# Optimization experiments

Measured on AMD Instinct MI355X. Metric: run time of the kernel, lower is better.

The kernel has to match this reference:

```python
import jax, jax.numpy as jnp
import numpy as np


def setup_inputs() -> dict:
    key = jax.random.key(0)
    k1, k2, k3, k4, k5 = jax.random.split(key, 5)
    B, S, T = 256, 512, 64
    emissions = jax.random.normal(k1, (B, S, T), dtype=jnp.float32)
    tags = jax.random.randint(k2, (B, S), 0, T, dtype=jnp.int64)
    mask = jnp.ones((B, S), dtype=jnp.int32)
    init_range = 0.1
    start_transitions = jax.random.uniform(k3, (T,), minval=-init_range, maxval=init_range, dtype=jnp.float32)
    end_transitions = jax.random.uniform(k4, (T,), minval=-init_range, maxval=init_range, dtype=jnp.float32)
    transitions = jax.random.uniform(k5, (T, T), minval=-init_range, maxval=init_range, dtype=jnp.float32)
    return {"emissions": emissions, "tags": tags, "mask": mask,
            "start_transitions": start_transitions,
            "end_transitions": end_transitions,
            "transitions": transitions}


def _crf_nll_mean(emissions, tags, mask, start_transitions, end_transitions, transitions):
    # batch_first -> time-major: [S, B, T], [S, B]
    em = jnp.transpose(emissions, (1, 0, 2))
    tg = jnp.transpose(tags, (1, 0))
    mk = jnp.transpose(mask, (1, 0))
    maskf = mk.astype(em.dtype)                      # [S, B]
    S, B, T = em.shape
    batch_idx = jnp.arange(B)

    # ---- numerator: score of the gold path (fully vectorized) ----
    emit = jnp.take_along_axis(em, tg[:, :, None], axis=2)[..., 0]   # [S, B]
    trans_sc = transitions[tg[:-1], tg[1:]]                          # [S-1, B]
    score_num = start_transitions[tg[0]] + emit[0]
    score_num = score_num + jnp.sum((trans_sc + emit[1:]) * maskf[1:], axis=0)
    seq_ends = jnp.sum(mk, axis=0) - 1                               # [B]
    last_tags = tg[seq_ends, batch_idx]
    score_num = score_num + end_transitions[last_tags]

    # ---- denominator: log-partition via logsumexp scan ----
    init = start_transitions + em[0]                                 # [B, T]

    def step(score, xs):
        em_i, m_i = xs                                               # [B,T], [B]
        # [B, T_prev, T_next]
        next_score = score[:, :, None] + transitions[None, :, :] + em_i[:, None, :]
        next_score = jax.nn.logsumexp(next_score, axis=1)
        score = jnp.where(m_i[:, None] != 0, next_score, score)
        return score, None

    final, _ = jax.lax.scan(step, init, (em[1:], mk[1:]))
    denom = jax.nn.logsumexp(final + end_transitions, axis=1)        # [B]

    llh = denom - score_num                                          # [B]
    return jnp.mean(llh)                                             # reduction='mean'


def reference(emissions, tags, mask, start_transitions, end_transitions, transitions):
    return _crf_nll_mean(emissions, tags, mask, start_transitions, end_transitions, transitions)
```

## Files before the change

### kernel.cpp

```cpp
#include <hip/hip_runtime.h>
#include <hip/hip_bf16.h>

#define BATCH 256
#define SEQ   512
#define NT    64
#define PCH   12
#define CLEN  43
#define PITCH 68

typedef __attribute__((ext_vector_type(8)))  short bf16x8;
typedef __attribute__((ext_vector_type(16))) float f32x16;
typedef __attribute__((ext_vector_type(4)))  float f32x4;

#define MEMBAR() __asm__ __volatile__("" ::: "memory")

static __device__ __forceinline__ short bf16_trunc(float v) {
    return (short)(__float_as_uint(v) >> 16);
}
static __device__ __forceinline__ unsigned pack_bf16_rn(float lo, float hi) {
    float2 f; f.x = lo; f.y = hi;
    __hip_bfloat162 h = __float22bfloat162_rn(f);
    unsigned u; __builtin_memcpy(&u, &h, 4);
    return u;
}

__global__ __launch_bounds__(64, 2) void crf_chunk_kernel(
    const float* __restrict__ emissions,
    const int*   __restrict__ tags,
    const int*   __restrict__ mask,
    const float* __restrict__ start_tr,
    const float* __restrict__ trans,
    unsigned short* __restrict__ mats,
    float* __restrict__ ws_head,
    float* __restrict__ score_part,
    int*   __restrict__ mcnt_part)
{
    __shared__ __align__(16) unsigned char smem[CLEN * NT * 4];
    float (*w_lds)[NT] = (float (*)[NT])smem;
    unsigned short* ldsT = (unsigned short*)smem;

    const int c    = blockIdx.x;
    const int b    = blockIdx.y;
    const int lane = threadIdx.x;
    const int h    = lane >> 5;
    const int ml   = lane & 31;

    if (c == 0 && b == 0 && lane == 0) {
        ws_head[0] = 0.f;
        ((unsigned*)ws_head)[1] = 0u;
    }

    const int s0 = c * CLEN;
    int L = (SEQ - 1) - s0; if (L > CLEN) L = CLEN;

    const float* em_b = emissions + (size_t)b * SEQ * NT;
    const int*   tg_b = tags + b * SEQ;
    const int*   mk_b = mask + b * SEQ;

    for (int s = 0; s < L; ++s)
        w_lds[s][lane] = __expf(em_b[(size_t)(s0 + 1 + s) * NT + lane]);

    float np = 0.f;
    int   mc = 0;
    if (lane < L) {
        int s  = s0 + 1 + lane;
        int m  = mk_b[s];
        mc = m;
        int t  = tg_b[s];
        int tp = tg_b[s - 1];
        float v = trans[tp * NT + t] + em_b[(size_t)s * NT + t];
        np = m ? v : 0.f;
    }
    if (c == 0 && lane == 0) {
        int t0 = tg_b[0];
        np += start_tr[t0] + em_b[t0];
        mc += mk_b[0];
    }
#pragma unroll
    for (int d = 32; d; d >>= 1) {
        np += __shfl_xor(np, d);
        mc += __shfl_xor(mc, d);
    }
    if (lane == 0) {
        score_part[b * PCH + c] = np;
        mcnt_part[b * PCH + c]  = mc;
    }

    bf16x8 Af[2][4];
#pragma unroll
    for (int mt = 0; mt < 2; ++mt) {
        int m = mt * 32 + ml;
#pragma unroll
        for (int kk = 0; kk < 4; ++kk) {
            bf16x8 f;
#pragma unroll
            for (int j = 0; j < 8; ++j) {
                int r = 32 * (kk >> 1) + 16 * (kk & 1) + (j & 3) + 8 * (j >> 2) + 4 * h;
                f[j] = bf16_trunc(__expf(trans[r * NT + m]) * 0.0078125f);
            }
            Af[mt][kk] = f;
        }
    }

    union BU { unsigned u[4]; bf16x8 v; };
    BU Bv[4][2];
#pragma unroll
    for (int kk = 0; kk < 4; ++kk)
#pragma unroll
        for (int nt = 0; nt < 2; ++nt) {
            int n = nt * 32 + ml;
#pragma unroll
            for (int d = 0; d < 4; ++d) {
                int j0 = 2 * d;
                int r0 = 32 * (kk >> 1) + 16 * (kk & 1) + (j0 & 3) + 8 * (j0 >> 2) + 4 * h;
                unsigned lo = (r0     == n) ? 0x3f80u : 0u;
                unsigned hi = (r0 + 1 == n) ? 0x3f80u : 0u;
                Bv[kk][nt].u[d] = lo | (hi << 16);
            }
        }

    __syncthreads();

    const f32x16 zf = {};

    for (int s = 0; s < L; ++s) {
        f32x4 wq[4][2];
#pragma unroll
        for (int kk = 0; kk < 4; ++kk) {
            int base = 32 * (kk >> 1) + 16 * (kk & 1) + 4 * h;
            wq[kk][0] = *(const f32x4*)&w_lds[s][base];
            wq[kk][1] = *(const f32x4*)&w_lds[s][base + 8];
        }

        f32x16 acc[2][2];
#pragma unroll
        for (int mt = 0; mt < 2; ++mt)
#pragma unroll
            for (int nt = 0; nt < 2; ++nt) {
                f32x16 a = __builtin_amdgcn_mfma_f32_32x32x16_bf16(Af[mt][0], Bv[0][nt].v, zf, 0, 0, 0);
                a = __builtin_amdgcn_mfma_f32_32x32x16_bf16(Af[mt][1], Bv[1][nt].v, a, 0, 0, 0);
                a = __builtin_amdgcn_mfma_f32_32x32x16_bf16(Af[mt][2], Bv[2][nt].v, a, 0, 0, 0);
                a = __builtin_amdgcn_mfma_f32_32x32x16_bf16(Af[mt][3], Bv[3][nt].v, a, 0, 0, 0);
                acc[mt][nt] = a;
            }

#pragma unroll
        for (int kk = 0; kk < 4; ++kk) {
            const int mt_s = kk >> 1, qo = 8 * (kk & 1);
#pragma unroll
            for (int nt = 0; nt < 2; ++nt) {
#pragma unroll
                for (int d = 0; d < 4; ++d) {
                    int j0 = 2 * d;
                    float v0 = acc[mt_s][nt][qo + j0]     * wq[kk][d >> 1][2 * (d & 1)];
                    float v1 = acc[mt_s][nt][qo + j0 + 1] * wq[kk][d >> 1][2 * (d & 1) + 1];
                    Bv[kk][nt].u[d] = pack_bf16_rn(v0, v1);
                }
            }
        }
    }

    __threadfence_block();
#pragma unroll
    for (int kk = 0; kk < 4; ++kk)
#pragma unroll
        for (int nt = 0; nt < 2; ++nt) {
            int n = nt * 32 + ml;
#pragma unroll
            for (int d = 0; d < 4; ++d) {
                int j0 = 2 * d;
                int r0 = 32 * (kk >> 1) + 16 * (kk & 1) + (j0 & 3) + 8 * (j0 >> 2) + 4 * h;
                *(unsigned*)&ldsT[n * PITCH + r0] = Bv[kk][nt].u[d];
            }
        }
    __threadfence_block();

    unsigned short* outp = mats + ((size_t)(b * PCH + c)) * 4096;
    for (int it = 0; it < 8; ++it) {
        int o = it * 512 + lane * 8;
        int n = o >> 6, k = o & 63;
        const uint2* p = (const uint2*)(ldsT + n * PITCH + k);
        uint2 x = p[0], y = p[1];
        uint4 q4; q4.x = x.x; q4.y = x.y; q4.z = y.x; q4.w = y.y;
        *(uint4*)(outp + o) = q4;
    }
}

__global__ __launch_bounds__(64) void crf_combine_kernel(
    const float* __restrict__ emissions,
    const int*   __restrict__ tags,
    const float* __restrict__ start_tr,
    const float* __restrict__ end_tr,
    const unsigned short* __restrict__ mats,
    const float* __restrict__ score_part,
    const int*   __restrict__ mcnt_part,
    float* __restrict__ ws_head,
    float* __restrict__ out)
{
    __shared__ __align__(16) float r_lds[NT];

    const int b = blockIdx.x;
    const int j = threadIdx.x;

    const float* em_b = emissions + (size_t)b * SEQ * NT;
    const int*   tg_b = tags + b * SEQ;
    const unsigned short* mb = mats + (size_t)b * PCH * 4096;

    float sp = (j < PCH) ? score_part[b * PCH + j] : 0.f;
    int   mp = (j < PCH) ? mcnt_part[b * PCH + j] : 0;

    float r = __expf(end_tr[j]);
    r_lds[j] = r;
    MEMBAR();
    int X = 0;

    uint4 buf[3][8];
#pragma unroll
    for (int u = 0; u < 8; ++u)
        buf[0][u] = *(const uint4*)(mb + (size_t)(PCH - 1) * 4096 + j * 64 + u * 8);
#pragma unroll
    for (int u = 0; u < 8; ++u)
        buf[1][u] = *(const uint4*)(mb + (size_t)(PCH - 2) * 4096 + j * 64 + u * 8);

#pragma unroll
    for (int d = 32; d; d >>= 1) {
        sp += __shfl_xor(sp, d);
        mp += __shfl_xor(mp, d);
    }
    int last_tag = tg_b[mp - 1];
    float score_num = sp + end_tr[last_tag];

#pragma unroll
    for (int c = PCH - 1; c >= 0; --c) {
        const int slot  = (PCH - 1 - c) % 3;
        const int nslot = (PCH - 1 - c + 2) % 3;
        if (c >= 2) {
#pragma unroll
            for (int u = 0; u < 8; ++u)
                buf[nslot][u] = *(const uint4*)(mb + (size_t)(c - 2) * 4096 + j * 64 + u * 8);
        }
        float a0 = 0.f, a1 = 0.f, a2 = 0.f, a3 = 0.f;
#pragma unroll
        for (int u = 0; u < 8; ++u) {
            uint4 q = buf[slot][u];
            f32x4 ra = *(const f32x4*)&r_lds[u * 8];
            f32x4 rb = *(const f32x4*)&r_lds[u * 8 + 4];
            a0 = fmaf(ra[0], __uint_as_float(q.x << 16),         a0);
            a1 = fmaf(ra[1], __uint_as_float(q.x & 0xffff0000u), a1);
            a2 = fmaf(ra[2], __uint_as_float(q.y << 16),         a2);
            a3 = fmaf(ra[3], __uint_as_float(q.y & 0xffff0000u), a3);
            a0 = fmaf(rb[0], __uint_as_float(q.z << 16),         a0);
            a1 = fmaf(rb[1], __uint_as_float(q.z & 0xffff0000u), a1);
            a2 = fmaf(rb[2], __uint_as_float(q.w << 16),         a2);
            a3 = fmaf(rb[3], __uint_as_float(q.w & 0xffff0000u), a3);
        }
        float rn = (a0 + a1) + (a2 + a3);
        unsigned eb = (__builtin_amdgcn_readfirstlane((int)__float_as_uint(rn)) >> 23) & 0xffu;
        r = rn * __uint_as_float((254u - eb) << 23);
        X += (int)eb - 127;
        MEMBAR();
        r_lds[j] = r;
        MEMBAR();
    }

    float u0 = __expf(start_tr[j] + em_b[j]);
    float v = r * u0;
#pragma unroll
    for (int d = 32; d; d >>= 1) v += __shfl_xor(v, d);

    if (j == 0) {
        float denom = __logf(v) + (float)(X + 7 * (SEQ - 1)) * 0.6931471805599453f;
        float llh = denom - score_num;
        atomicAdd(&ws_head[0], llh * (1.0f / BATCH));
        __threadfence();
        unsigned old = atomicAdd((unsigned*)ws_head + 1, 1u);
        if (old == BATCH - 1) {
            __threadfence();
            out[0] = atomicAdd(&ws_head[0], 0.0f);
        }
    }
}

extern "C" void kernel_launch(void* const* d_in, const int* in_sizes, int n_in,
                              void* d_out, int out_size, void* d_ws, size_t ws_size,
                              hipStream_t stream) {
    const float* emissions = (const float*)d_in[0];
    const int*   tags      = (const int*)d_in[1];
    const int*   mask      = (const int*)d_in[2];
    const float* start_tr  = (const float*)d_in[3];
    const float* end_tr    = (const float*)d_in[4];
    const float* trans     = (const float*)d_in[5];

    float* ws_head    = (float*)d_ws;
    float* score_part = (float*)((char*)d_ws + 64);
    int*   mcnt_part  = (int*)((char*)d_ws + 64 + 4 * BATCH * PCH);
    unsigned short* mats = (unsigned short*)((char*)d_ws + 32768);

    crf_chunk_kernel<<<dim3(PCH, BATCH), 64, 0, stream>>>(
        emissions, tags, mask, start_tr, trans, mats, ws_head, score_part, mcnt_part);
    crf_combine_kernel<<<BATCH, 64, 0, stream>>>(
        emissions, tags, start_tr, end_tr, mats, score_part, mcnt_part,
        ws_head, (float*)d_out);
}
```

Measured before the change: 166.8 us.

## Fuse chunk and combine kernels via last-block atomic, split columns across two waves

Merges the per-chunk matrix-product kernel and the combine kernel into one launch. The last block to finish for each batch row, detected with an atomic counter that a memset clears, does the combine. Each block now runs two waves, each owning half the output columns, which halves the serial MFMA chain per wave. Chunk count drops from 12 to 8 with longer chunks. This removes a kernel launch and boundary, but the dependent chain per block gets longer, and it adds a memset plus global fences.

```diff
diff --git a/kernel.cpp b/kernel.cpp
--- a/kernel.cpp
+++ b/kernel.cpp
@@ -4,13 +4,13 @@
 #define BATCH 256
 #define SEQ   512
 #define NT    64
-#define PCH   12
-#define CLEN  43
+#define PCH   8
+#define CLEN  64
 #define PITCH 68
 
-typedef __attribute__((ext_vector_type(8)))  short bf16x8;
-typedef __attribute__((ext_vector_type(16))) float f32x16;
-typedef __attribute__((ext_vector_type(4)))  float f32x4;
+typedef short bf16x8  __attribute__((ext_vector_type(8)));
+typedef float f32x16  __attribute__((ext_vector_type(16)));
+typedef float f32x4   __attribute__((ext_vector_type(4)));
 
 #define MEMBAR() __asm__ __volatile__("" ::: "memory")
 
@@ -19,36 +19,38 @@
 }
 static __device__ __forceinline__ unsigned pack_bf16_rn(float lo, float hi) {
     float2 f; f.x = lo; f.y = hi;
-    __hip_bfloat162 h = __float22bfloat162_rn(f);
-    unsigned u; __builtin_memcpy(&u, &h, 4);
+    __hip_bfloat162 hh = __float22bfloat162_rn(f);
+    unsigned u; __builtin_memcpy(&u, &hh, 4);
     return u;
 }
 
-__global__ __launch_bounds__(64, 2) void crf_chunk_kernel(
+__global__ __launch_bounds__(128, 4) void crf_fused_kernel(
     const float* __restrict__ emissions,
     const int*   __restrict__ tags,
     const int*   __restrict__ mask,
     const float* __restrict__ start_tr,
+    const float* __restrict__ end_tr,
     const float* __restrict__ trans,
     unsigned short* __restrict__ mats,
     float* __restrict__ ws_head,
+    unsigned* __restrict__ done,
     float* __restrict__ score_part,
-    int*   __restrict__ mcnt_part)
+    int*   __restrict__ mcnt_part,
+    float* __restrict__ out)
 {
     __shared__ __align__(16) unsigned char smem[CLEN * NT * 4];
+    __shared__ unsigned is_last;
     float (*w_lds)[NT] = (float (*)[NT])smem;
     unsigned short* ldsT = (unsigned short*)smem;
+    float* r_lds = (float*)smem;
 
     const int c    = blockIdx.x;
     const int b    = blockIdx.y;
-    const int lane = threadIdx.x;
+    const int tid  = threadIdx.x;
+    const int lane = tid & 63;
+    const int wave = tid >> 6;
     const int h    = lane >> 5;
     const int ml   = lane & 31;
-
-    if (c == 0 && b == 0 && lane == 0) {
-        ws_head[0] = 0.f;
-        ((unsigned*)ws_head)[1] = 0u;
-    }
 
     const int s0 = c * CLEN;
     int L = (SEQ - 1) - s0; if (L > CLEN) L = CLEN;
@@ -57,33 +59,35 @@
     const int*   tg_b = tags + b * SEQ;
     const int*   mk_b = mask + b * SEQ;
 
-    for (int s = 0; s < L; ++s)
-        w_lds[s][lane] = __expf(em_b[(size_t)(s0 + 1 + s) * NT + lane]);
-
-    float np = 0.f;
-    int   mc = 0;
-    if (lane < L) {
-        int s  = s0 + 1 + lane;
-        int m  = mk_b[s];
-        mc = m;
-        int t  = tg_b[s];
-        int tp = tg_b[s - 1];
-        float v = trans[tp * NT + t] + em_b[(size_t)s * NT + t];
-        np = m ? v : 0.f;
-    }
-    if (c == 0 && lane == 0) {
-        int t0 = tg_b[0];
-        np += start_tr[t0] + em_b[t0];
-        mc += mk_b[0];
-    }
-#pragma unroll
-    for (int d = 32; d; d >>= 1) {
-        np += __shfl_xor(np, d);
-        mc += __shfl_xor(mc, d);
-    }
-    if (lane == 0) {
-        score_part[b * PCH + c] = np;
-        mcnt_part[b * PCH + c]  = mc;
+    for (int i = tid; i < L * NT; i += 128)
+        ((float*)smem)[i] = __expf(em_b[(size_t)(s0 + 1) * NT + i]);
+
+    if (wave == 0) {
+        float np = 0.f;
+        int   mc = 0;
+        if (lane < L) {
+            int s  = s0 + 1 + lane;
+            int m  = mk_b[s];
+            mc = m;
+            int t  = tg_b[s];
+            int tp = tg_b[s - 1];
+            float v = trans[tp * NT + t] + em_b[(size_t)s * NT + t];
+            np = m ? v : 0.f;
+        }
+        if (c == 0 && lane == 0) {
+            int t0 = tg_b[0];
+            np += start_tr[t0] + em_b[t0];
+            mc += mk_b[0];
+        }
+#pragma unroll
+        for (int d = 32; d; d >>= 1) {
+            np += __shfl_xor(np, d);
+            mc += __shfl_xor(mc, d);
+        }
+        if (lane == 0) {
+            score_part[b * PCH + c] = np;
+            mcnt_part[b * PCH + c]  = mc;
+        }
     }
 
     bf16x8 Af[2][4];
@@ -103,141 +107,116 @@
     }
 
     union BU { unsigned u[4]; bf16x8 v; };
-    BU Bv[4][2];
+    BU Bv[4];
+    const int n_own = wave * 32 + ml;
 #pragma unroll
     for (int kk = 0; kk < 4; ++kk)
 #pragma unroll
-        for (int nt = 0; nt < 2; ++nt) {
-            int n = nt * 32 + ml;
+        for (int d = 0; d < 4; ++d) {
+            int j0 = 2 * d;
+            int r0 = 32 * (kk >> 1) + 16 * (kk & 1) + (j0 & 3) + 8 * (j0 >> 2) + 4 * h;
+            unsigned lo = (r0     == n_own) ? 0x3f80u : 0u;
+            unsigned hi = (r0 + 1 == n_own) ? 0x3f80u : 0u;
+            Bv[kk].u[d] = lo | (hi << 16);
+        }
+
+    __syncthreads();
+
+    for (int s = 0; s < L; ++s) {
+        f32x4 wq0[4], wq1[4];
+#pragma unroll
+        for (int kk = 0; kk < 4; ++kk) {
+            int base = 32 * (kk >> 1) + 16 * (kk & 1) + 4 * h;
+            wq0[kk] = *(const f32x4*)&w_lds[s][base];
+            wq1[kk] = *(const f32x4*)&w_lds[s][base + 8];
+        }
+
+        const f32x16 zf = {};
+        f32x16 a0 = __builtin_amdgcn_mfma_f32_32x32x16_bf16(Af[0][0], Bv[0].v, zf, 0, 0, 0);
+        a0 = __builtin_amdgcn_mfma_f32_32x32x16_bf16(Af[0][1], Bv[1].v, a0, 0, 0, 0);
+        a0 = __builtin_amdgcn_mfma_f32_32x32x16_bf16(Af[0][2], Bv[2].v, a0, 0, 0, 0);
+        a0 = __builtin_amdgcn_mfma_f32_32x32x16_bf16(Af[0][3], Bv[3].v, a0, 0, 0, 0);
+        f32x16 a1 = __builtin_amdgcn_mfma_f32_32x32x16_bf16(Af[1][0], Bv[0].v, zf, 0, 0, 0);
+        a1 = __builtin_amdgcn_mfma_f32_32x32x16_bf16(Af[1][1], Bv[1].v, a1, 0, 0, 0);
+        a1 = __builtin_amdgcn_mfma_f32_32x32x16_bf16(Af[1][2], Bv[2].v, a1, 0, 0, 0);
+        a1 = __builtin_amdgcn_mfma_f32_32x32x16_bf16(Af[1][3], Bv[3].v, a1, 0, 0, 0);
+
+#pragma unroll
+        for (int kk = 0; kk < 4; ++kk) {
+            const int qo = 8 * (kk & 1);
 #pragma unroll
             for (int d = 0; d < 4; ++d) {
                 int j0 = 2 * d;
-                int r0 = 32 * (kk >> 1) + 16 * (kk & 1) + (j0 & 3) + 8 * (j0 >> 2) + 4 * h;
-                unsigned lo = (r0     == n) ? 0x3f80u : 0u;
-                unsigned hi = (r0 + 1 == n) ? 0x3f80u : 0u;
-                Bv[kk][nt].u[d] = lo | (hi << 16);
+                float c0 = (kk < 2) ? a0[qo + j0]     : a1[qo + j0];
+                float c1 = (kk < 2) ? a0[qo + j0 + 1] : a1[qo + j0 + 1];
+                float w0 = (d < 2) ? wq0[kk][2 * (d & 1)]     : wq1[kk][2 * (d & 1)];
+                float w1 = (d < 2) ? wq0[kk][2 * (d & 1) + 1] : wq1[kk][2 * (d & 1) + 1];
+                Bv[kk].u[d] = pack_bf16_rn(c0 * w0, c1 * w1);
             }
         }
-
-    __syncthreads();
-
-    const f32x16 zf = {};
-
-    for (int s = 0; s < L; ++s) {
-        f32x4 wq[4][2];
-#pragma unroll
-        for (int kk = 0; kk < 4; ++kk) {
-            int base = 32 * (kk >> 1) + 16 * (kk & 1) + 4 * h;
-            wq[kk][0] = *(const f32x4*)&w_lds[s][base];
-            wq[kk][1] = *(const f32x4*)&w_lds[s][base + 8];
-        }
-
-        f32x16 acc[2][2];
-#pragma unroll
-        for (int mt = 0; mt < 2; ++mt)
-#pragma unroll
-            for (int nt = 0; nt < 2; ++nt) {
-                f32x16 a = __builtin_amdgcn_mfma_f32_32x32x16_bf16(Af[mt][0], Bv[0][nt].v, zf, 0, 0, 0);
-                a = __builtin_amdgcn_mfma_f32_32x32x16_bf16(Af[mt][1], Bv[1][nt].v, a, 0, 0, 0);
-                a = __builtin_amdgcn_mfma_f32_32x32x16_bf16(Af[mt][2], Bv[2][nt].v, a, 0, 0, 0);
-                a = __builtin_amdgcn_mfma_f32_32x32x16_bf16(Af[mt][3], Bv[3][nt].v, a, 0, 0, 0);
-                acc[mt][nt] = a;
-            }
-
-#pragma unroll
-        for (int kk = 0; kk < 4; ++kk) {
-            const int mt_s = kk >> 1, qo = 8 * (kk & 1);
-#pragma unroll
-            for (int nt = 0; nt < 2; ++nt) {
-#pragma unroll
-                for (int d = 0; d < 4; ++d) {
-                    int j0 = 2 * d;
-                    float v0 = acc[mt_s][nt][qo + j0]     * wq[kk][d >> 1][2 * (d & 1)];
-                    float v1 = acc[mt_s][nt][qo + j0 + 1] * wq[kk][d >> 1][2 * (d & 1) + 1];
-                    Bv[kk][nt].u[d] = pack_bf16_rn(v0, v1);
-                }
-            }
-        }
-    }
-
-    __threadfence_block();
+    }
+
+    __syncthreads();
 #pragma unroll
     for (int kk = 0; kk < 4; ++kk)
 #pragma unroll
-        for (int nt = 0; nt < 2; ++nt) {
-            int n = nt * 32 + ml;
-#pragma unroll
-            for (int d = 0; d < 4; ++d) {
-                int j0 = 2 * d;
-                int r0 = 32 * (kk >> 1) + 16 * (kk & 1) + (j0 & 3) + 8 * (j0 >> 2) + 4 * h;
-                *(unsigned*)&ldsT[n * PITCH + r0] = Bv[kk][nt].u[d];
-            }
-        }
-    __threadfence_block();
+        for (int d = 0; d < 4; ++d) {
+            int j0 = 2 * d;
+            int r0 = 32 * (kk >> 1) + 16 * (kk & 1) + (j0 & 3) + 8 * (j0 >> 2) + 4 * h;
+            *(unsigned*)&ldsT[n_own * PITCH + r0] = Bv[kk].u[d];
+        }
+    __syncthreads();
 
     unsigned short* outp = mats + ((size_t)(b * PCH + c)) * 4096;
-    for (int it = 0; it < 8; ++it) {
-        int o = it * 512 + lane * 8;
+    for (int it = 0; it < 4; ++it) {
+        int o = it * 1024 + tid * 8;
         int n = o >> 6, k = o & 63;
         const uint2* p = (const uint2*)(ldsT + n * PITCH + k);
         uint2 x = p[0], y = p[1];
         uint4 q4; q4.x = x.x; q4.y = x.y; q4.z = y.x; q4.w = y.y;
         *(uint4*)(outp + o) = q4;
     }
-}
-
-__global__ __launch_bounds__(64) void crf_combine_kernel(
-    const float* __restrict__ emissions,
-    const int*   __restrict__ tags,
-    const float* __restrict__ start_tr,
-    const float* __restrict__ end_tr,
-    const unsigned short* __restrict__ mats,
-    const float* __restrict__ score_part,
-    const int*   __restrict__ mcnt_part,
-    float* __restrict__ ws_head,
-    float* __restrict__ out)
-{
-    __shared__ __align__(16) float r_lds[NT];
-
-    const int b = blockIdx.x;
-    const int j = threadIdx.x;
-
-    const float* em_b = emissions + (size_t)b * SEQ * NT;
-    const int*   tg_b = tags + b * SEQ;
+
+    __threadfence();
+    __syncthreads();
+    if (tid == 0) {
+        unsigned old = atomicAdd(&done[b], 1u);
+        is_last = (old == PCH - 1) ? 1u : 0u;
+    }
+    __syncthreads();
+    if (!is_last) return;
+    __threadfence();
+    if (wave != 0) return;
+
+    const int j = lane;
     const unsigned short* mb = mats + (size_t)b * PCH * 4096;
 
     float sp = (j < PCH) ? score_part[b * PCH + j] : 0.f;
     int   mp = (j < PCH) ? mcnt_part[b * PCH + j] : 0;
 
     float r = __expf(end_tr[j]);
-    r_lds[j] = r;
-    MEMBAR();
+    MEMBAR(); r_lds[j] = r; MEMBAR();
     int X = 0;
 
-    uint4 buf[3][8];
+    uint4 buf[2][8];
 #pragma unroll
     for (int u = 0; u < 8; ++u)
         buf[0][u] = *(const uint4*)(mb + (size_t)(PCH - 1) * 4096 + j * 64 + u * 8);
-#pragma unroll
-    for (int u = 0; u < 8; ++u)
-        buf[1][u] = *(const uint4*)(mb + (size_t)(PCH - 2) * 4096 + j * 64 + u * 8);
 
 #pragma unroll
     for (int d = 32; d; d >>= 1) {
         sp += __shfl_xor(sp, d);
         mp += __shfl_xor(mp, d);
     }
-    int last_tag = tg_b[mp - 1];
-    float score_num = sp + end_tr[last_tag];
-
-#pragma unroll
-    for (int c = PCH - 1; c >= 0; --c) {
-        const int slot  = (PCH - 1 - c) % 3;
-        const int nslot = (PCH - 1 - c + 2) % 3;
-        if (c >= 2) {
+    float score_num = sp + end_tr[tg_b[mp - 1]];
+
+#pragma unroll
+    for (int cc = PCH - 1; cc >= 0; --cc) {
+        const int slot = (PCH - 1 - cc) & 1;
+        if (cc > 0) {
 #pragma unroll
             for (int u = 0; u < 8; ++u)
-                buf[nslot][u] = *(const uint4*)(mb + (size_t)(c - 2) * 4096 + j * 64 + u * 8);
+                buf[slot ^ 1][u] = *(const uint4*)(mb + (size_t)(cc - 1) * 4096 + j * 64 + u * 8);
         }
         float a0 = 0.f, a1 = 0.f, a2 = 0.f, a3 = 0.f;
 #pragma unroll
@@ -291,14 +270,14 @@
     const float* end_tr    = (const float*)d_in[4];
     const float* trans     = (const float*)d_in[5];
 
-    float* ws_head    = (float*)d_ws;
-    float* score_part = (float*)((char*)d_ws + 64);
-    int*   mcnt_part  = (int*)((char*)d_ws + 64 + 4 * BATCH * PCH);
+    float*    ws_head    = (float*)d_ws;
+    unsigned* done       = (unsigned*)((char*)d_ws + 64);
+    float*    score_part = (float*)((char*)d_ws + 4096);
+    int*      mcnt_part  = (int*)((char*)d_ws + 12288);
     unsigned short* mats = (unsigned short*)((char*)d_ws + 32768);
 
-    crf_chunk_kernel<<<dim3(PCH, BATCH), 64, 0, stream>>>(
-        emissions, tags, mask, start_tr, trans, mats, ws_head, score_part, mcnt_part);
-    crf_combine_kernel<<<BATCH, 64, 0, stream>>>(
-        emissions, tags, start_tr, end_tr, mats, score_part, mcnt_part,
-        ws_head, (float*)d_out);
-}
+    hipMemsetAsync(d_ws, 0, 4096, stream);
+    crf_fused_kernel<<<dim3(PCH, BATCH), 128, 0, stream>>>(
+        emissions, tags, mask, start_tr, end_tr, trans,
+        mats, ws_head, done, score_part, mcnt_part, (float*)d_out);
+}
```

New measurement: 300.8 us. 1.8x slower.

## Fuse chunk and combine kernels via last-block-done counter, use 8 chunks

Applied to the files above, without the earlier changes.

Merges the per-chunk transfer-matrix kernel and the combine kernel into one launch. The last chunk block of each batch row, detected with an atomic counter, performs the chain of matrix-vector products. Chunk length grows from 43 to 64, so there are 8 chunks instead of 12 and the combine chain is shorter, at the cost of longer per-block sequential work. A memset is added to zero the counters, and the combine prefetch buffer drops from triple to double.

```diff
diff --git a/kernel.cpp b/kernel.cpp
--- a/kernel.cpp
+++ b/kernel.cpp
@@ -4,13 +4,13 @@
 #define BATCH 256
 #define SEQ   512
 #define NT    64
-#define PCH   12
-#define CLEN  43
+#define PCH   8
+#define CLEN  64
 #define PITCH 68
 
-typedef __attribute__((ext_vector_type(8)))  short bf16x8;
-typedef __attribute__((ext_vector_type(16))) float f32x16;
-typedef __attribute__((ext_vector_type(4)))  float f32x4;
+typedef short bf16x8  __attribute__((ext_vector_type(8)));
+typedef float f32x16  __attribute__((ext_vector_type(16)));
+typedef float f32x4   __attribute__((ext_vector_type(4)));
 
 #define MEMBAR() __asm__ __volatile__("" ::: "memory")
 
@@ -19,25 +19,29 @@
 }
 static __device__ __forceinline__ unsigned pack_bf16_rn(float lo, float hi) {
     float2 f; f.x = lo; f.y = hi;
-    __hip_bfloat162 h = __float22bfloat162_rn(f);
-    unsigned u; __builtin_memcpy(&u, &h, 4);
+    __hip_bfloat162 hh = __float22bfloat162_rn(f);
+    unsigned u; __builtin_memcpy(&u, &hh, 4);
     return u;
 }
 
-__global__ __launch_bounds__(64, 2) void crf_chunk_kernel(
+__global__ __launch_bounds__(64, 2) void crf_fused_kernel(
     const float* __restrict__ emissions,
     const int*   __restrict__ tags,
     const int*   __restrict__ mask,
     const float* __restrict__ start_tr,
+    const float* __restrict__ end_tr,
     const float* __restrict__ trans,
     unsigned short* __restrict__ mats,
     float* __restrict__ ws_head,
+    unsigned* __restrict__ done,
     float* __restrict__ score_part,
-    int*   __restrict__ mcnt_part)
+    int*   __restrict__ mcnt_part,
+    float* __restrict__ out)
 {
     __shared__ __align__(16) unsigned char smem[CLEN * NT * 4];
     float (*w_lds)[NT] = (float (*)[NT])smem;
     unsigned short* ldsT = (unsigned short*)smem;
+    float* r_lds = (float*)smem;
 
     const int c    = blockIdx.x;
     const int b    = blockIdx.y;
@@ -45,11 +49,6 @@
     const int h    = lane >> 5;
     const int ml   = lane & 31;
 
-    if (c == 0 && b == 0 && lane == 0) {
-        ws_head[0] = 0.f;
-        ((unsigned*)ws_head)[1] = 0u;
-    }
-
     const int s0 = c * CLEN;
     int L = (SEQ - 1) - s0; if (L > CLEN) L = CLEN;
 
@@ -60,30 +59,32 @@
     for (int s = 0; s < L; ++s)
         w_lds[s][lane] = __expf(em_b[(size_t)(s0 + 1 + s) * NT + lane]);
 
-    float np = 0.f;
-    int   mc = 0;
-    if (lane < L) {
-        int s  = s0 + 1 + lane;
-        int m  = mk_b[s];
-        mc = m;
-        int t  = tg_b[s];
-        int tp = tg_b[s - 1];
-        float v = trans[tp * NT + t] + em_b[(size_t)s * NT + t];
-        np = m ? v : 0.f;
-    }
-    if (c == 0 && lane == 0) {
-        int t0 = tg_b[0];
-        np += start_tr[t0] + em_b[t0];
-        mc += mk_b[0];
-    }
-#pragma unroll
-    for (int d = 32; d; d >>= 1) {
-        np += __shfl_xor(np, d);
-        mc += __shfl_xor(mc, d);
-    }
-    if (lane == 0) {
-        score_part[b * PCH + c] = np;
-        mcnt_part[b * PCH + c]  = mc;
+    {
+        float np = 0.f;
+        int   mc = 0;
+        if (lane < L) {
+            int s  = s0 + 1 + lane;
+            int m  = mk_b[s];
+            mc = m;
+            int t  = tg_b[s];
+            int tp = tg_b[s - 1];
+            float v = trans[tp * NT + t] + em_b[(size_t)s * NT + t];
+            np = m ? v : 0.f;
+        }
+        if (c == 0 && lane == 0) {
+            int t0 = tg_b[0];
+            np += start_tr[t0] + em_b[t0];
+            mc += mk_b[0];
+        }
+#pragma unroll
+        for (int d = 32; d; d >>= 1) {
+            np += __shfl_xor(np, d);
+            mc += __shfl_xor(mc, d);
+        }
+        if (lane == 0) {
+            score_part[b * PCH + c] = np;
+            mcnt_part[b * PCH + c]  = mc;
+        }
     }
 
     bf16x8 Af[2][4];
@@ -184,60 +185,43 @@
         uint4 q4; q4.x = x.x; q4.y = x.y; q4.z = y.x; q4.w = y.y;
         *(uint4*)(outp + o) = q4;
     }
-}
-
-__global__ __launch_bounds__(64) void crf_combine_kernel(
-    const float* __restrict__ emissions,
-    const int*   __restrict__ tags,
-    const float* __restrict__ start_tr,
-    const float* __restrict__ end_tr,
-    const unsigned short* __restrict__ mats,
-    const float* __restrict__ score_part,
-    const int*   __restrict__ mcnt_part,
-    float* __restrict__ ws_head,
-    float* __restrict__ out)
-{
-    __shared__ __align__(16) float r_lds[NT];
-
-    const int b = blockIdx.x;
-    const int j = threadIdx.x;
-
-    const float* em_b = emissions + (size_t)b * SEQ * NT;
-    const int*   tg_b = tags + b * SEQ;
+
+    __threadfence();
+    unsigned old = 0;
+    if (lane == 0) old = atomicAdd(&done[b], 1u);
+    old = __shfl(old, 0);
+    if (old != PCH - 1) return;
+    __threadfence();
+
+    const int j = lane;
     const unsigned short* mb = mats + (size_t)b * PCH * 4096;
 
     float sp = (j < PCH) ? score_part[b * PCH + j] : 0.f;
     int   mp = (j < PCH) ? mcnt_part[b * PCH + j] : 0;
 
     float r = __expf(end_tr[j]);
-    r_lds[j] = r;
-    MEMBAR();
+    MEMBAR(); r_lds[j] = r; MEMBAR();
     int X = 0;
 
-    uint4 buf[3][8];
+    uint4 buf[2][8];
 #pragma unroll
     for (int u = 0; u < 8; ++u)
         buf[0][u] = *(const uint4*)(mb + (size_t)(PCH - 1) * 4096 + j * 64 + u * 8);
-#pragma unroll
-    for (int u = 0; u < 8; ++u)
-        buf[1][u] = *(const uint4*)(mb + (size_t)(PCH - 2) * 4096 + j * 64 + u * 8);
 
 #pragma unroll
     for (int d = 32; d; d >>= 1) {
         sp += __shfl_xor(sp, d);
         mp += __shfl_xor(mp, d);
     }
-    int last_tag = tg_b[mp - 1];
-    float score_num = sp + end_tr[last_tag];
-
-#pragma unroll
-    for (int c = PCH - 1; c >= 0; --c) {
-        const int slot  = (PCH - 1 - c) % 3;
-        const int nslot = (PCH - 1 - c + 2) % 3;
-        if (c >= 2) {
+    float score_num = sp + end_tr[tg_b[mp - 1]];
+
+#pragma unroll
+    for (int cc = PCH - 1; cc >= 0; --cc) {
+        const int slot = (PCH - 1 - cc) & 1;
+        if (cc > 0) {
 #pragma unroll
             for (int u = 0; u < 8; ++u)
-                buf[nslot][u] = *(const uint4*)(mb + (size_t)(c - 2) * 4096 + j * 64 + u * 8);
+                buf[slot ^ 1][u] = *(const uint4*)(mb + (size_t)(cc - 1) * 4096 + j * 64 + u * 8);
         }
         float a0 = 0.f, a1 = 0.f, a2 = 0.f, a3 = 0.f;
 #pragma unroll
@@ -273,8 +257,8 @@
         float llh = denom - score_num;
         atomicAdd(&ws_head[0], llh * (1.0f / BATCH));
         __threadfence();
-        unsigned old = atomicAdd((unsigned*)ws_head + 1, 1u);
-        if (old == BATCH - 1) {
+        unsigned oldc = atomicAdd((unsigned*)ws_head + 1, 1u);
+        if (oldc == BATCH - 1) {
             __threadfence();
             out[0] = atomicAdd(&ws_head[0], 0.0f);
         }
@@ -291,14 +275,14 @@
     const float* end_tr    = (const float*)d_in[4];
     const float* trans     = (const float*)d_in[5];
 
-    float* ws_head    = (float*)d_ws;
-    float* score_part = (float*)((char*)d_ws + 64);
-    int*   mcnt_part  = (int*)((char*)d_ws + 64 + 4 * BATCH * PCH);
+    float*    ws_head    = (float*)d_ws;
+    unsigned* done       = (unsigned*)((char*)d_ws + 64);
+    float*    score_part = (float*)((char*)d_ws + 4096);
+    int*      mcnt_part  = (int*)((char*)d_ws + 12288);
     unsigned short* mats = (unsigned short*)((char*)d_ws + 32768);
 
-    crf_chunk_kernel<<<dim3(PCH, BATCH), 64, 0, stream>>>(
-        emissions, tags, mask, start_tr, trans, mats, ws_head, score_part, mcnt_part);
-    crf_combine_kernel<<<BATCH, 64, 0, stream>>>(
-        emissions, tags, start_tr, end_tr, mats, score_part, mcnt_part,
-        ws_head, (float*)d_out);
-}
+    hipMemsetAsync(d_ws, 0, 4096, stream);
+    crf_fused_kernel<<<dim3(PCH, BATCH), 64, 0, stream>>>(
+        emissions, tags, mask, start_tr, end_tr, trans,
+        mats, ws_head, done, score_part, mcnt_part, (float*)d_out);
+}
```

After: 233.5 us. 1.4x slower.
